# Kernel tuning notes

Measured on AMD Instinct MI355X. Metric: run time of the kernel, lower is better.

The kernel has to match this reference:

```python
import jax, jax.numpy as jnp
import numpy as np
from jax import lax

D_STATE = 16
D_CONV = 4
EXPAND = 2


def setup_inputs() -> dict:
    key = jax.random.key(0)
    ks = jax.random.split(key, 12)
    B, C, H, W = 8, 192, 32, 32
    d_inner = EXPAND * C            # 384
    dt_rank = (C + 15) // 16        # 12
    s = lambda k, shape, sc=0.02: jax.random.normal(k, shape, jnp.float32) * sc
    return {
        "x": jax.random.normal(ks[0], (B, C, H, W), jnp.float32),
        # proj_in: 1x1 Conv2d (in_ch -> out_ch)
        "proj_w": s(ks[1], (C, C)),
        "proj_b": s(ks[2], (C,)),
        # Mamba params (mamba_ssm defaults, biases per reference impl)
        "in_proj_w": s(ks[3], (2 * d_inner, C)),
        "conv_w": s(ks[4], (d_inner, D_CONV)),
        "conv_b": s(ks[5], (d_inner,)),
        "xproj_w": s(ks[6], (dt_rank + 2 * D_STATE, d_inner)),
        "dtproj_w": s(ks[7], (d_inner, dt_rank), 0.1),
        "dtproj_b": s(ks[8], (d_inner,), 0.5),
        "A_log": jnp.log(jnp.tile(jnp.arange(1, D_STATE + 1, dtype=jnp.float32), (d_inner, 1))),
        "Dp": jnp.ones((d_inner,), jnp.float32),
        "out_w": s(ks[9], (C, d_inner)),
    }


def _forward(x, proj_w, proj_b, in_proj_w, conv_w, conv_b, xproj_w,
             dtproj_w, dtproj_b, A_log, Dp, out_w):
    B, C, H, W = x.shape
    L = H * W
    # proj_in (1x1 conv) + flatten 'b c h w -> b (h w) c'
    u = jnp.einsum('bchw,oc->bhwo', x, proj_w).reshape(B, L, -1) + proj_b
    # Mamba layer
    xz = u @ in_proj_w.T                      # [B,L,2*d_inner]
    xin, z = jnp.split(xz, 2, axis=-1)
    # causal depthwise conv1d (kernel D_CONV), truncated to L
    xp = jnp.pad(xin, ((0, 0), (D_CONV - 1, 0), (0, 0)))
    xc = conv_b + sum(conv_w[:, k] * xp[:, k:k + L, :] for k in range(D_CONV))
    xc = jax.nn.silu(xc)
    # input-dependent dt, B, C
    dt_rank = dtproj_w.shape[1]
    x_dbl = xc @ xproj_w.T                    # [B,L,dt_rank+2*n]
    dtr, Bt, Ct = jnp.split(x_dbl, [dt_rank, dt_rank + D_STATE], axis=-1)
    dt = jax.nn.softplus(dtr @ dtproj_w.T + dtproj_b)   # [B,L,d_inner]
    A = -jnp.exp(A_log)                       # [d_inner, n]
    deltaA = jnp.exp(dt[..., None] * A)                          # [B,L,d,n]
    dBx = dt[..., None] * Bt[:, :, None, :] * xc[..., None]      # [B,L,d,n]

    def step(h, ins):
        dA, dbx, ct = ins                      # [B,d,n],[B,d,n],[B,n]
        h = dA * h + dbx
        return h, jnp.einsum('bdn,bn->bd', h, ct)

    h0 = jnp.zeros((B, A.shape[0], D_STATE), xc.dtype)
    _, ys = lax.scan(step, h0, (deltaA.transpose(1, 0, 2, 3),
                                dBx.transpose(1, 0, 2, 3),
                                Ct.transpose(1, 0, 2)))
    y = ys.transpose(1, 0, 2) + xc * Dp        # [B,L,d_inner]
    y = y * jax.nn.silu(z)
    out = y @ out_w.T                          # [B,L,C]
    # 'b (h w) c -> b c h w'
    return out.reshape(B, H, W, C).transpose(0, 3, 1, 2)


def reference(x, proj_w, proj_b, in_proj_w, conv_w, conv_b, xproj_w,
              dtproj_w, dtproj_b, A_log, Dp, out_w):
    return _forward(x, proj_w, proj_b, in_proj_w, conv_w, conv_b, xproj_w,
                    dtproj_w, dtproj_b, A_log, Dp, out_w)
```

## Files before the change

### kernel.cpp

```cpp
#include <hip/hip_runtime.h>
#include <math.h>

#define BB 8
#define CC 192
#define LL 1024
#define RT 8192
#define DI 384
#define DT_RANK 12
#define NS 16
#define NSEG 16
#define SEGL 64

typedef __attribute__((ext_vector_type(8))) short bf16x8;
typedef __attribute__((ext_vector_type(4))) float f32x4;

__device__ __forceinline__ unsigned short f2bf(float f) {
    unsigned u = __float_as_uint(f);
    unsigned r = (u + 0x7FFFu + ((u >> 16) & 1u)) >> 16;
    return (unsigned short)r;
}
__device__ __forceinline__ float bf2f(unsigned short h) {
    return __uint_as_float(((unsigned)h) << 16);
}

__device__ __forceinline__ float row_sum16(float v) {
    v += __int_as_float(__builtin_amdgcn_update_dpp(0, __float_as_int(v), 0x140, 0xF, 0xF, true));
    v += __int_as_float(__builtin_amdgcn_update_dpp(0, __float_as_int(v), 0x141, 0xF, 0xF, true));
    v += __int_as_float(__builtin_amdgcn_update_dpp(0, __float_as_int(v), 0x4E,  0xF, 0xF, true));
    v += __int_as_float(__builtin_amdgcn_update_dpp(0, __float_as_int(v), 0xB1,  0xF, 0xF, true));
    return v;
}

__global__ void fuse_w_kernel(const float* __restrict__ in_proj_w,
                              const float* __restrict__ proj_w,
                              const float* __restrict__ proj_b,
                              const float* __restrict__ out_w,
                              unsigned short* __restrict__ W2hi,
                              unsigned short* __restrict__ W2lo,
                              unsigned short* __restrict__ owhi,
                              unsigned short* __restrict__ owlo,
                              float* __restrict__ bias2,
                              float* __restrict__ xdT) {
    int j = blockIdx.x;
    int cp = threadIdx.x;
    int gtid = j * CC + cp;
    for (int i = gtid; i < 44 * RT; i += 768 * CC) xdT[i] = 0.f;
    if (j < DI) {
        float v = out_w[cp * DI + j];
        unsigned short h = f2bf(v);
        owhi[cp * DI + j] = h;
        owlo[cp * DI + j] = f2bf(v - bf2f(h));
    }
    __shared__ float wrow[CC];
    wrow[cp] = in_proj_w[j * CC + cp];
    __syncthreads();
    float acc = 0.f;
#pragma unroll 4
    for (int c = 0; c < CC; ++c) acc = fmaf(wrow[c], proj_w[c * CC + cp], acc);
    unsigned short h = f2bf(acc);
    W2hi[j * CC + cp] = h;
    W2lo[j * CC + cp] = f2bf(acc - bf2f(h));
    if (cp == 0) {
        float b = 0.f;
        for (int c = 0; c < CC; ++c) b = fmaf(wrow[c], proj_b[c], b);
        bias2[j] = b;
    }
}

__global__ __launch_bounds__(256) void gemm_xz(const float* __restrict__ x,
                                               const unsigned short* __restrict__ W2hi,
                                               const unsigned short* __restrict__ W2lo,
                                               const float* __restrict__ bias2,
                                               float* __restrict__ xzT) {
    __shared__ unsigned short xhi[2048];
    __shared__ unsigned short xlo[2048];
    int r0 = blockIdx.x * 64;
    int j0 = blockIdx.y * 64;
    int b  = r0 >> 10;
    int l0 = r0 & 1023;
    int tid = threadIdx.x;
    int lane = tid & 63;
    int wid = tid >> 6;
    int jw = j0 + wid * 16;
    const float* xb = x + b * CC * LL + l0 + lane;
    f32x4 z4 = {0.f, 0.f, 0.f, 0.f};
    f32x4 acc[4] = {z4, z4, z4, z4};
    int arow = jw + (lane & 15);
    int akb  = (lane >> 4) * 8;
    for (int ks = 0; ks < 6; ++ks) {
        int k0 = ks * 32;
        float v[8];
#pragma unroll
        for (int e = 0; e < 8; ++e) v[e] = xb[(k0 + wid * 8 + e) * LL];
        union U8 { unsigned short u[8]; bf16x8 v8; } hv, lv;
#pragma unroll
        for (int e = 0; e < 8; ++e) {
            unsigned short h = f2bf(v[e]);
            hv.u[e] = h;
            lv.u[e] = f2bf(v[e] - bf2f(h));
        }
        *(bf16x8*)&xhi[(wid * 64 + lane) * 8] = hv.v8;
        *(bf16x8*)&xlo[(wid * 64 + lane) * 8] = lv.v8;
        __syncthreads();
        int aoff = arow * CC + k0 + akb;
        bf16x8 ah = *(const bf16x8*)&W2hi[aoff];
        bf16x8 al = *(const bf16x8*)&W2lo[aoff];
#pragma unroll
        for (int rt = 0; rt < 4; ++rt) {
            int boff = ((lane >> 4) * 64 + rt * 16 + (lane & 15)) * 8;
            bf16x8 bh = *(const bf16x8*)&xhi[boff];
            bf16x8 bl = *(const bf16x8*)&xlo[boff];
            acc[rt] = __builtin_amdgcn_mfma_f32_16x16x32_bf16(ah, bh, acc[rt], 0, 0, 0);
            acc[rt] = __builtin_amdgcn_mfma_f32_16x16x32_bf16(ah, bl, acc[rt], 0, 0, 0);
            acc[rt] = __builtin_amdgcn_mfma_f32_16x16x32_bf16(al, bh, acc[rt], 0, 0, 0);
        }
        __syncthreads();
    }
    bool is_z = (j0 >= DI);
#pragma unroll
    for (int rt = 0; rt < 4; ++rt) {
        int rbase = r0 + rt * 16 + (lane & 15);
#pragma unroll
        for (int reg = 0; reg < 4; ++reg) {
            int j = jw + (lane >> 4) * 4 + reg;
            float o = acc[rt][reg] + bias2[j];
            if (is_z) o = __fdividef(o, 1.f + __expf(-o));
            xzT[j * RT + rbase] = o;
        }
    }
}

__global__ __launch_bounds__(512) void xproj_conv_gemm(const float* __restrict__ xzT,
                                                       const float* __restrict__ conv_w,
                                                       const float* __restrict__ conv_b,
                                                       const float* __restrict__ aw,
                                                       float* __restrict__ xcT,
                                                       float* __restrict__ xdT) {
    __shared__ float Bs[32][64];
    int col0 = blockIdx.x * 64;
    int kbase = blockIdx.y * 192;
    int tid = threadIdx.x;
    int col = tid & 63, mg = tid >> 6;
    int mb = mg * 6;
    const float* ar[6];
#pragma unroll
    for (int m = 0; m < 6; ++m) ar[m] = aw + min(mb + m, 43) * DI + kbase;
    float acc[6] = {};
    int ks = tid >> 4, c4 = (tid & 15) * 4;
    bool atL0 = ((col0 & 1023) == 0) && (c4 == 0);
    for (int k0 = 0; k0 < 192; k0 += 32) {
        int dch = kbase + k0 + ks;
        const float* src = xzT + (size_t)dch * RT + col0 + c4;
        float4 cur = *(const float4*)src;
        float4 prev = make_float4(0.f, 0.f, 0.f, 0.f);
        if (!atL0) prev = *(const float4*)(src - 4);
        float4 w4 = *(const float4*)&conv_w[dch * 4];
        float bb = conv_b[dch];
        float v0 = bb + w4.w * cur.x + w4.z * prev.w + w4.y * prev.z + w4.x * prev.y;
        float v1 = bb + w4.w * cur.y + w4.z * cur.x  + w4.y * prev.w + w4.x * prev.z;
        float v2 = bb + w4.w * cur.z + w4.z * cur.y  + w4.y * cur.x  + w4.x * prev.w;
        float v3 = bb + w4.w * cur.w + w4.z * cur.z  + w4.y * cur.y  + w4.x * cur.x;
        float4 o;
        o.x = __fdividef(v0, 1.f + __expf(-v0));
        o.y = __fdividef(v1, 1.f + __expf(-v1));
        o.z = __fdividef(v2, 1.f + __expf(-v2));
        o.w = __fdividef(v3, 1.f + __expf(-v3));
        *(float4*)&Bs[ks][c4] = o;
        *(float4*)&xcT[(size_t)dch * RT + col0 + c4] = o;
        __syncthreads();
#pragma unroll
        for (int k = 0; k < 32; ++k) {
            float bv = Bs[k][col];
#pragma unroll
            for (int m = 0; m < 6; ++m)
                acc[m] = fmaf(ar[m][k0 + k], bv, acc[m]);
        }
        __syncthreads();
    }
#pragma unroll
    for (int m = 0; m < 6; ++m)
        if (mb + m < 44)
            atomicAdd(&xdT[(mb + m) * RT + col0 + col], acc[m]);
}

__global__ __launch_bounds__(256) void scan_part1(const float* __restrict__ xdT,
                                                  const float* __restrict__ xcT,
                                                  const float* __restrict__ dtw,
                                                  const float* __restrict__ dtb,
                                                  const float* __restrict__ A_log,
                                                  float* __restrict__ P,
                                                  float* __restrict__ Hf) {
    __shared__ float dt_s[16][20], g_s[16][20], B_s[16][20];
    __shared__ float dtr_s[12][17];
    __shared__ float dtw_s[192];
    __shared__ float dtb_s[16];
    int seg = blockIdx.x, d0 = blockIdx.y * 16, b = blockIdx.z;
    int row0 = b * LL + seg * SEGL;
    int tid = threadIdx.x;
    int lane = tid & 63;
    int n = lane & 15;
    int dl = ((tid >> 6) << 2) | (lane >> 4);
    int tdd = tid >> 4, ti = tid & 15;
    if (tid < 192) dtw_s[tid] = dtw[d0 * DT_RANK + tid];
    if (tid < 16)  dtb_s[tid] = dtb[d0 + tid];
    float a = -__expf(A_log[(d0 + dl) * NS + n]);
    float h = 0.f, sdt = 0.f;
    for (int ch = 0; ch < 4; ++ch) {
        int r = row0 + ch * 16;
        float xv = xcT[(d0 + tdd) * RT + r + ti];
        B_s[tdd][ti] = xdT[(12 + tdd) * RT + r + ti];
        if (tid < 192) dtr_s[tid >> 4][ti] = xdT[(tid >> 4) * RT + r + ti];
        __syncthreads();
        float acc = dtb_s[tdd];
#pragma unroll
        for (int rr = 0; rr < DT_RANK; ++rr)
            acc = fmaf(dtr_s[rr][ti], dtw_s[tdd * DT_RANK + rr], acc);
        float dtv = fmaxf(acc, 0.f) + __logf(1.f + __expf(-fabsf(acc)));
        dt_s[tdd][ti] = dtv;
        g_s[tdd][ti]  = dtv * xv;
        __syncthreads();
        float dv[16], gb[16];
#pragma unroll
        for (int q = 0; q < 4; ++q) {
            float4 d4 = *(const float4*)&dt_s[dl][q * 4];
            float4 g4 = *(const float4*)&g_s[dl][q * 4];
            float4 b4 = *(const float4*)&B_s[n][q * 4];
            dv[q * 4 + 0] = d4.x; dv[q * 4 + 1] = d4.y;
            dv[q * 4 + 2] = d4.z; dv[q * 4 + 3] = d4.w;
            gb[q * 4 + 0] = g4.x * b4.x; gb[q * 4 + 1] = g4.y * b4.y;
            gb[q * 4 + 2] = g4.z * b4.z; gb[q * 4 + 3] = g4.w * b4.w;
        }
        __syncthreads();
        float eh[16];
#pragma unroll
        for (int i = 0; i < 16; ++i) eh[i] = __expf(dv[i] * a);
#pragma unroll
        for (int i = 0; i < 16; ++i) {
            sdt += dv[i];
            h = fmaf(eh[i], h, gb[i]);
        }
    }
    int idx = ((seg * BB + b) * DI + d0 + dl) * NS + n;
    P[idx] = __expf(a * sdt);
    Hf[idx] = h;
}

__global__ __launch_bounds__(256) void scan_part2(const float* __restrict__ xdT,
                                                  const float* __restrict__ xcT,
                                                  const float* __restrict__ zsT,
                                                  const float* __restrict__ dtw,
                                                  const float* __restrict__ dtb,
                                                  const float* __restrict__ P,
                                                  const float* __restrict__ Hf,
                                                  const float* __restrict__ A_log,
                                                  const float* __restrict__ Dp,
                                                  float* __restrict__ yT) {
    __shared__ float dt_s[16][20], g_s[16][20], B_s[16][20], C_s[16][20];
    __shared__ float dtr_s[12][17];
    __shared__ float dtw_s[192];
    __shared__ float dtb_s[16];
    int seg = blockIdx.x, d0 = blockIdx.y * 16, b = blockIdx.z;
    int row0 = b * LL + seg * SEGL;
    int tid = threadIdx.x;
    int lane = tid & 63;
    int n = lane & 15;
    int dl = ((tid >> 6) << 2) | (lane >> 4);
    int d = d0 + dl;
    int tdd = tid >> 4, ti = tid & 15;
    if (tid < 192) dtw_s[tid] = dtw[d0 * DT_RANK + tid];
    if (tid < 16)  dtb_s[tid] = dtb[d0 + tid];
    float a = -__expf(A_log[d * NS + n]);
    float Dpd = Dp[d];
    float h = 0.f;
    for (int s = 0; s < seg; ++s) {
        int off = ((s * BB + b) * DI + d) * NS + n;
        h = fmaf(P[off], h, Hf[off]);
    }
    for (int ch = 0; ch < 4; ++ch) {
        int r = row0 + ch * 16;
        float xr = xcT[(size_t)d * RT + r + n];
        float zr = zsT[(size_t)d * RT + r + n];
        float xv = xcT[(d0 + tdd) * RT + r + ti];
        B_s[tdd][ti] = xdT[(12 + tdd) * RT + r + ti];
        C_s[tdd][ti] = xdT[(28 + tdd) * RT + r + ti];
        if (tid < 192) dtr_s[tid >> 4][ti] = xdT[(tid >> 4) * RT + r + ti];
        __syncthreads();
        float acc = dtb_s[tdd];
#pragma unroll
        for (int rr = 0; rr < DT_RANK; ++rr)
            acc = fmaf(dtr_s[rr][ti], dtw_s[tdd * DT_RANK + rr], acc);
        float dtv = fmaxf(acc, 0.f) + __logf(1.f + __expf(-fabsf(acc)));
        dt_s[tdd][ti] = dtv;
        g_s[tdd][ti]  = dtv * xv;
        __syncthreads();
        float dv[16], gb[16], cv[16];
#pragma unroll
        for (int q = 0; q < 4; ++q) {
            float4 d4 = *(const float4*)&dt_s[dl][q * 4];
            float4 g4 = *(const float4*)&g_s[dl][q * 4];
            float4 b4 = *(const float4*)&B_s[n][q * 4];
            float4 c4 = *(const float4*)&C_s[n][q * 4];
            dv[q * 4 + 0] = d4.x; dv[q * 4 + 1] = d4.y;
            dv[q * 4 + 2] = d4.z; dv[q * 4 + 3] = d4.w;
            gb[q * 4 + 0] = g4.x * b4.x; gb[q * 4 + 1] = g4.y * b4.y;
            gb[q * 4 + 2] = g4.z * b4.z; gb[q * 4 + 3] = g4.w * b4.w;
            cv[q * 4 + 0] = c4.x; cv[q * 4 + 1] = c4.y;
            cv[q * 4 + 2] = c4.z; cv[q * 4 + 3] = c4.w;
        }
        __syncthreads();
        float eh[16];
#pragma unroll
        for (int i = 0; i < 16; ++i) eh[i] = __expf(dv[i] * a);
        float yacc = 0.f;
#pragma unroll
        for (int i = 0; i < 16; ++i) {
            h = fmaf(eh[i], h, gb[i]);
            float v = row_sum16(h * cv[i]);
            yacc = (n == i) ? v : yacc;
        }
        yT[(size_t)d * RT + r + n] = fmaf(xr, Dpd, yacc) * zr;
    }
}

__global__ __launch_bounds__(256) void gemm_out(const float* __restrict__ yT,
                                                const unsigned short* __restrict__ owhi,
                                                const unsigned short* __restrict__ owlo,
                                                float* __restrict__ out) {
    __shared__ unsigned short yhi[2048];
    __shared__ unsigned short ylo[2048];
    int r0 = blockIdx.x * 64;
    int c0 = blockIdx.y * 64;
    int b  = r0 >> 10;
    int l0 = r0 & 1023;
    int tid = threadIdx.x;
    int lane = tid & 63;
    int wid = tid >> 6;
    int cw = c0 + wid * 16;
    const float* yb = yT + r0 + lane;
    f32x4 z4 = {0.f, 0.f, 0.f, 0.f};
    f32x4 acc[4] = {z4, z4, z4, z4};
    int arow = cw + (lane & 15);
    int akb  = (lane >> 4) * 8;
    for (int ks = 0; ks < 12; ++ks) {
        int k0 = ks * 32;
        float v[8];
#pragma unroll
        for (int e = 0; e < 8; ++e) v[e] = yb[(size_t)(k0 + wid * 8 + e) * RT];
        union U8 { unsigned short u[8]; bf16x8 v8; } hv, lv;
#pragma unroll
        for (int e = 0; e < 8; ++e) {
            unsigned short h = f2bf(v[e]);
            hv.u[e] = h;
            lv.u[e] = f2bf(v[e] - bf2f(h));
        }
        *(bf16x8*)&yhi[(wid * 64 + lane) * 8] = hv.v8;
        *(bf16x8*)&ylo[(wid * 64 + lane) * 8] = lv.v8;
        __syncthreads();
        int aoff = arow * DI + k0 + akb;
        bf16x8 ah = *(const bf16x8*)&owhi[aoff];
        bf16x8 al = *(const bf16x8*)&owlo[aoff];
#pragma unroll
        for (int rt = 0; rt < 4; ++rt) {
            int boff = ((lane >> 4) * 64 + rt * 16 + (lane & 15)) * 8;
            bf16x8 bh = *(const bf16x8*)&yhi[boff];
            bf16x8 bl = *(const bf16x8*)&ylo[boff];
            acc[rt] = __builtin_amdgcn_mfma_f32_16x16x32_bf16(ah, bh, acc[rt], 0, 0, 0);
            acc[rt] = __builtin_amdgcn_mfma_f32_16x16x32_bf16(ah, bl, acc[rt], 0, 0, 0);
            acc[rt] = __builtin_amdgcn_mfma_f32_16x16x32_bf16(al, bh, acc[rt], 0, 0, 0);
        }
        __syncthreads();
    }
    float* ob = out + b * CC * LL;
#pragma unroll
    for (int rt = 0; rt < 4; ++rt) {
        int lbase = l0 + rt * 16 + (lane & 15);
#pragma unroll
        for (int reg = 0; reg < 4; ++reg) {
            int c = cw + (lane >> 4) * 4 + reg;
            ob[c * LL + lbase] = acc[rt][reg];
        }
    }
}

extern "C" void kernel_launch(void* const* d_in, const int* in_sizes, int n_in,
                              void* d_out, int out_size, void* d_ws, size_t ws_size,
                              hipStream_t stream) {
    const float* x         = (const float*)d_in[0];
    const float* proj_w    = (const float*)d_in[1];
    const float* proj_b    = (const float*)d_in[2];
    const float* in_proj_w = (const float*)d_in[3];
    const float* conv_w    = (const float*)d_in[4];
    const float* conv_b    = (const float*)d_in[5];
    const float* xproj_w   = (const float*)d_in[6];
    const float* dtproj_w  = (const float*)d_in[7];
    const float* dtproj_b  = (const float*)d_in[8];
    const float* A_log     = (const float*)d_in[9];
    const float* Dp        = (const float*)d_in[10];
    const float* out_w     = (const float*)d_in[11];
    float* out = (float*)d_out;

    float* ws    = (float*)d_ws;
    unsigned short* W2hi = (unsigned short*)ws;
    unsigned short* W2lo = (unsigned short*)(ws + 73728);
    float* bias2 = ws + 147456;
    float* xzT   = bias2 + 768;
    float* xcT   = xzT + 6291456;
    float* yT    = xcT + 3145728;
    float* xdT   = yT + 3145728;
    float* P     = xdT + 360448;
    float* Hf    = P + 786432;
    unsigned short* owhi = (unsigned short*)(Hf + 786432);
    unsigned short* owlo = (unsigned short*)(Hf + 786432 + 36864);
    float* zsT   = xzT + DI * RT;

    fuse_w_kernel<<<768, 192, 0, stream>>>(in_proj_w, proj_w, proj_b, out_w,
                                           W2hi, W2lo, owhi, owlo, bias2, xdT);
    gemm_xz<<<dim3(128, 12), 256, 0, stream>>>(x, W2hi, W2lo, bias2, xzT);
    xproj_conv_gemm<<<dim3(128, 2), 512, 0, stream>>>(xzT, conv_w, conv_b,
                                                      xproj_w, xcT, xdT);
    scan_part1<<<dim3(16, 24, 8), 256, 0, stream>>>(xdT, xcT, dtproj_w, dtproj_b,
                                                    A_log, P, Hf);
    scan_part2<<<dim3(16, 24, 8), 256, 0, stream>>>(xdT, xcT, zsT, dtproj_w, dtproj_b,
                                                    P, Hf, A_log, Dp, yT);
    gemm_out<<<dim3(128, 3), 256, 0, stream>>>(yT, owhi, owlo, out);
}
```

Measured before the change: 202.2 us.

## Replace two-pass segmented scan with single-pass sequential scan with register prefetch

Merges the segmented two-kernel selective scan into one kernel where each block scans the full sequence for 16 channels of one batch, dropping the per-segment state/decay intermediates and the recomputation in the first pass. Next-chunk inputs are prefetched into registers to hide global load latency, and one barrier per chunk is removed. This trades away segment-level parallelism, leaving only 192 blocks with a long serial dependency chain per block.

```diff
diff --git a/kernel.cpp b/kernel.cpp
--- a/kernel.cpp
+++ b/kernel.cpp
@@ -8,8 +8,6 @@
 #define DI 384
 #define DT_RANK 12
 #define NS 16
-#define NSEG 16
-#define SEGL 64
 
 typedef __attribute__((ext_vector_type(8))) short bf16x8;
 typedef __attribute__((ext_vector_type(4))) float f32x4;
@@ -183,84 +181,20 @@
             atomicAdd(&xdT[(mb + m) * RT + col0 + col], acc[m]);
 }
 
-__global__ __launch_bounds__(256) void scan_part1(const float* __restrict__ xdT,
-                                                  const float* __restrict__ xcT,
-                                                  const float* __restrict__ dtw,
-                                                  const float* __restrict__ dtb,
-                                                  const float* __restrict__ A_log,
-                                                  float* __restrict__ P,
-                                                  float* __restrict__ Hf) {
-    __shared__ float dt_s[16][20], g_s[16][20], B_s[16][20];
-    __shared__ float dtr_s[12][17];
-    __shared__ float dtw_s[192];
-    __shared__ float dtb_s[16];
-    int seg = blockIdx.x, d0 = blockIdx.y * 16, b = blockIdx.z;
-    int row0 = b * LL + seg * SEGL;
-    int tid = threadIdx.x;
-    int lane = tid & 63;
-    int n = lane & 15;
-    int dl = ((tid >> 6) << 2) | (lane >> 4);
-    int tdd = tid >> 4, ti = tid & 15;
-    if (tid < 192) dtw_s[tid] = dtw[d0 * DT_RANK + tid];
-    if (tid < 16)  dtb_s[tid] = dtb[d0 + tid];
-    float a = -__expf(A_log[(d0 + dl) * NS + n]);
-    float h = 0.f, sdt = 0.f;
-    for (int ch = 0; ch < 4; ++ch) {
-        int r = row0 + ch * 16;
-        float xv = xcT[(d0 + tdd) * RT + r + ti];
-        B_s[tdd][ti] = xdT[(12 + tdd) * RT + r + ti];
-        if (tid < 192) dtr_s[tid >> 4][ti] = xdT[(tid >> 4) * RT + r + ti];
-        __syncthreads();
-        float acc = dtb_s[tdd];
-#pragma unroll
-        for (int rr = 0; rr < DT_RANK; ++rr)
-            acc = fmaf(dtr_s[rr][ti], dtw_s[tdd * DT_RANK + rr], acc);
-        float dtv = fmaxf(acc, 0.f) + __logf(1.f + __expf(-fabsf(acc)));
-        dt_s[tdd][ti] = dtv;
-        g_s[tdd][ti]  = dtv * xv;
-        __syncthreads();
-        float dv[16], gb[16];
-#pragma unroll
-        for (int q = 0; q < 4; ++q) {
-            float4 d4 = *(const float4*)&dt_s[dl][q * 4];
-            float4 g4 = *(const float4*)&g_s[dl][q * 4];
-            float4 b4 = *(const float4*)&B_s[n][q * 4];
-            dv[q * 4 + 0] = d4.x; dv[q * 4 + 1] = d4.y;
-            dv[q * 4 + 2] = d4.z; dv[q * 4 + 3] = d4.w;
-            gb[q * 4 + 0] = g4.x * b4.x; gb[q * 4 + 1] = g4.y * b4.y;
-            gb[q * 4 + 2] = g4.z * b4.z; gb[q * 4 + 3] = g4.w * b4.w;
-        }
-        __syncthreads();
-        float eh[16];
-#pragma unroll
-        for (int i = 0; i < 16; ++i) eh[i] = __expf(dv[i] * a);
-#pragma unroll
-        for (int i = 0; i < 16; ++i) {
-            sdt += dv[i];
-            h = fmaf(eh[i], h, gb[i]);
-        }
-    }
-    int idx = ((seg * BB + b) * DI + d0 + dl) * NS + n;
-    P[idx] = __expf(a * sdt);
-    Hf[idx] = h;
-}
-
-__global__ __launch_bounds__(256) void scan_part2(const float* __restrict__ xdT,
-                                                  const float* __restrict__ xcT,
-                                                  const float* __restrict__ zsT,
-                                                  const float* __restrict__ dtw,
-                                                  const float* __restrict__ dtb,
-                                                  const float* __restrict__ P,
-                                                  const float* __restrict__ Hf,
-                                                  const float* __restrict__ A_log,
-                                                  const float* __restrict__ Dp,
-                                                  float* __restrict__ yT) {
+__global__ __launch_bounds__(256) void scan_full(const float* __restrict__ xdT,
+                                                 const float* __restrict__ xcT,
+                                                 const float* __restrict__ zsT,
+                                                 const float* __restrict__ dtw,
+                                                 const float* __restrict__ dtb,
+                                                 const float* __restrict__ A_log,
+                                                 const float* __restrict__ Dp,
+                                                 float* __restrict__ yT) {
     __shared__ float dt_s[16][20], g_s[16][20], B_s[16][20], C_s[16][20];
     __shared__ float dtr_s[12][17];
     __shared__ float dtw_s[192];
     __shared__ float dtb_s[16];
-    int seg = blockIdx.x, d0 = blockIdx.y * 16, b = blockIdx.z;
-    int row0 = b * LL + seg * SEGL;
+    int d0 = blockIdx.x * 16, b = blockIdx.y;
+    int row0 = b * LL;
     int tid = threadIdx.x;
     int lane = tid & 63;
     int n = lane & 15;
@@ -272,26 +206,34 @@
     float a = -__expf(A_log[d * NS + n]);
     float Dpd = Dp[d];
     float h = 0.f;
-    for (int s = 0; s < seg; ++s) {
-        int off = ((s * BB + b) * DI + d) * NS + n;
-        h = fmaf(P[off], h, Hf[off]);
-    }
-    for (int ch = 0; ch < 4; ++ch) {
+    float xv  = xcT[(d0 + tdd) * RT + row0 + ti];
+    float bvp = xdT[(12 + tdd) * RT + row0 + ti];
+    float cvp = xdT[(28 + tdd) * RT + row0 + ti];
+    float dtrv = (tid < 192) ? xdT[(tid >> 4) * RT + row0 + ti] : 0.f;
+    float xr = xcT[(size_t)d * RT + row0 + n];
+    float zr = zsT[(size_t)d * RT + row0 + n];
+    for (int ch = 0; ch < 64; ++ch) {
         int r = row0 + ch * 16;
-        float xr = xcT[(size_t)d * RT + r + n];
-        float zr = zsT[(size_t)d * RT + r + n];
-        float xv = xcT[(d0 + tdd) * RT + r + ti];
-        B_s[tdd][ti] = xdT[(12 + tdd) * RT + r + ti];
-        C_s[tdd][ti] = xdT[(28 + tdd) * RT + r + ti];
-        if (tid < 192) dtr_s[tid >> 4][ti] = xdT[(tid >> 4) * RT + r + ti];
-        __syncthreads();
+        __syncthreads();
+        B_s[tdd][ti] = bvp;
+        C_s[tdd][ti] = cvp;
+        if (tid < 192) dtr_s[tid >> 4][ti] = dtrv;
+        float xv_c = xv, xr_c = xr, zr_c = zr;
+        __syncthreads();
+        int rn = row0 + min(ch + 1, 63) * 16;
+        xv  = xcT[(d0 + tdd) * RT + rn + ti];
+        bvp = xdT[(12 + tdd) * RT + rn + ti];
+        cvp = xdT[(28 + tdd) * RT + rn + ti];
+        if (tid < 192) dtrv = xdT[(tid >> 4) * RT + rn + ti];
+        xr = xcT[(size_t)d * RT + rn + n];
+        zr = zsT[(size_t)d * RT + rn + n];
         float acc = dtb_s[tdd];
 #pragma unroll
         for (int rr = 0; rr < DT_RANK; ++rr)
             acc = fmaf(dtr_s[rr][ti], dtw_s[tdd * DT_RANK + rr], acc);
         float dtv = fmaxf(acc, 0.f) + __logf(1.f + __expf(-fabsf(acc)));
         dt_s[tdd][ti] = dtv;
-        g_s[tdd][ti]  = dtv * xv;
+        g_s[tdd][ti]  = dtv * xv_c;
         __syncthreads();
         float dv[16], gb[16], cv[16];
 #pragma unroll
@@ -307,7 +249,6 @@
             cv[q * 4 + 0] = c4.x; cv[q * 4 + 1] = c4.y;
             cv[q * 4 + 2] = c4.z; cv[q * 4 + 3] = c4.w;
         }
-        __syncthreads();
         float eh[16];
 #pragma unroll
         for (int i = 0; i < 16; ++i) eh[i] = __expf(dv[i] * a);
@@ -318,7 +259,7 @@
             float v = row_sum16(h * cv[i]);
             yacc = (n == i) ? v : yacc;
         }
-        yT[(size_t)d * RT + r + n] = fmaf(xr, Dpd, yacc) * zr;
+        yT[(size_t)d * RT + r + n] = fmaf(xr_c, Dpd, yacc) * zr_c;
     }
 }
 
@@ -407,10 +348,8 @@
     float* xcT   = xzT + 6291456;
     float* yT    = xcT + 3145728;
     float* xdT   = yT + 3145728;
-    float* P     = xdT + 360448;
-    float* Hf    = P + 786432;
-    unsigned short* owhi = (unsigned short*)(Hf + 786432);
-    unsigned short* owlo = (unsigned short*)(Hf + 786432 + 36864);
+    unsigned short* owhi = (unsigned short*)(xdT + 360448);
+    unsigned short* owlo = (unsigned short*)(xdT + 360448 + 36864);
     float* zsT   = xzT + DI * RT;
 
     fuse_w_kernel<<<768, 192, 0, stream>>>(in_proj_w, proj_w, proj_b, out_w,
@@ -418,9 +357,7 @@
     gemm_xz<<<dim3(128, 12), 256, 0, stream>>>(x, W2hi, W2lo, bias2, xzT);
     xproj_conv_gemm<<<dim3(128, 2), 512, 0, stream>>>(xzT, conv_w, conv_b,
                                                       xproj_w, xcT, xdT);
-    scan_part1<<<dim3(16, 24, 8), 256, 0, stream>>>(xdT, xcT, dtproj_w, dtproj_b,
-                                                    A_log, P, Hf);
-    scan_part2<<<dim3(16, 24, 8), 256, 0, stream>>>(xdT, xcT, zsT, dtproj_w, dtproj_b,
-                                                    P, Hf, A_log, Dp, yT);
+    scan_full<<<dim3(24, 8), 256, 0, stream>>>(xdT, xcT, zsT, dtproj_w, dtproj_b,
+                                               A_log, Dp, yT);
     gemm_out<<<dim3(128, 3), 256, 0, stream>>>(yT, owhi, owlo, out);
 }
```

New measurement: 218.9 us. 8.3% more time.

## Precompute dt and dt*x in separate kernel, drop shared-memory staging in scans

Applied to the files above, without the earlier changes.

Adds a dt_g_kernel that computes softplus(dt projection) and dt*xc once per element and writes them to global buffers dtT and gT. Both scan kernels then read dt, g, B and C directly from global memory with float4 loads instead of recomputing dt through shared memory, which removes their block-wide barriers. This avoids computing dt twice and the sync overhead in the scans, at the cost of an extra launch and about 25 MB of additional global writes and reads. The workspace layout is rearranged to hold the new buffers.

```diff
diff --git a/kernel.cpp b/kernel.cpp
--- a/kernel.cpp
+++ b/kernel.cpp
@@ -183,54 +183,67 @@
             atomicAdd(&xdT[(mb + m) * RT + col0 + col], acc[m]);
 }
 
-__global__ __launch_bounds__(256) void scan_part1(const float* __restrict__ xdT,
-                                                  const float* __restrict__ xcT,
-                                                  const float* __restrict__ dtw,
-                                                  const float* __restrict__ dtb,
+__global__ __launch_bounds__(256) void dt_g_kernel(const float* __restrict__ xdT,
+                                                   const float* __restrict__ xcT,
+                                                   const float* __restrict__ dtw,
+                                                   const float* __restrict__ dtb,
+                                                   float* __restrict__ dtT,
+                                                   float* __restrict__ gT) {
+    __shared__ float dtw_s[192];
+    __shared__ float dtb_s[16];
+    int tid = threadIdx.x;
+    int row = blockIdx.x * 256 + tid;
+    int d0 = blockIdx.y * 16;
+    if (tid < 192) dtw_s[tid] = dtw[d0 * DT_RANK + tid];
+    if (tid < 16)  dtb_s[tid] = dtb[d0 + tid];
+    __syncthreads();
+    float dtr[DT_RANK];
+#pragma unroll
+    for (int rr = 0; rr < DT_RANK; ++rr) dtr[rr] = xdT[rr * RT + row];
+#pragma unroll
+    for (int dd = 0; dd < 16; ++dd) {
+        int d = d0 + dd;
+        float acc = dtb_s[dd];
+#pragma unroll
+        for (int rr = 0; rr < DT_RANK; ++rr)
+            acc = fmaf(dtr[rr], dtw_s[dd * DT_RANK + rr], acc);
+        float dtv = fmaxf(acc, 0.f) + __logf(1.f + __expf(-fabsf(acc)));
+        dtT[(size_t)d * RT + row] = dtv;
+        gT[(size_t)d * RT + row]  = dtv * xcT[(size_t)d * RT + row];
+    }
+}
+
+__global__ __launch_bounds__(256) void scan_part1(const float* __restrict__ dtT,
+                                                  const float* __restrict__ gT,
+                                                  const float* __restrict__ xdT,
                                                   const float* __restrict__ A_log,
                                                   float* __restrict__ P,
                                                   float* __restrict__ Hf) {
-    __shared__ float dt_s[16][20], g_s[16][20], B_s[16][20];
-    __shared__ float dtr_s[12][17];
-    __shared__ float dtw_s[192];
-    __shared__ float dtb_s[16];
     int seg = blockIdx.x, d0 = blockIdx.y * 16, b = blockIdx.z;
     int row0 = b * LL + seg * SEGL;
     int tid = threadIdx.x;
     int lane = tid & 63;
     int n = lane & 15;
     int dl = ((tid >> 6) << 2) | (lane >> 4);
-    int tdd = tid >> 4, ti = tid & 15;
-    if (tid < 192) dtw_s[tid] = dtw[d0 * DT_RANK + tid];
-    if (tid < 16)  dtb_s[tid] = dtb[d0 + tid];
-    float a = -__expf(A_log[(d0 + dl) * NS + n]);
+    int d = d0 + dl;
+    float a = -__expf(A_log[d * NS + n]);
     float h = 0.f, sdt = 0.f;
     for (int ch = 0; ch < 4; ++ch) {
         int r = row0 + ch * 16;
-        float xv = xcT[(d0 + tdd) * RT + r + ti];
-        B_s[tdd][ti] = xdT[(12 + tdd) * RT + r + ti];
-        if (tid < 192) dtr_s[tid >> 4][ti] = xdT[(tid >> 4) * RT + r + ti];
-        __syncthreads();
-        float acc = dtb_s[tdd];
-#pragma unroll
-        for (int rr = 0; rr < DT_RANK; ++rr)
-            acc = fmaf(dtr_s[rr][ti], dtw_s[tdd * DT_RANK + rr], acc);
-        float dtv = fmaxf(acc, 0.f) + __logf(1.f + __expf(-fabsf(acc)));
-        dt_s[tdd][ti] = dtv;
-        g_s[tdd][ti]  = dtv * xv;
-        __syncthreads();
+        const float4* dt4 = (const float4*)&dtT[(size_t)d * RT + r];
+        const float4* g4p = (const float4*)&gT[(size_t)d * RT + r];
+        const float4* b4p = (const float4*)&xdT[(size_t)(12 + n) * RT + r];
         float dv[16], gb[16];
 #pragma unroll
         for (int q = 0; q < 4; ++q) {
-            float4 d4 = *(const float4*)&dt_s[dl][q * 4];
-            float4 g4 = *(const float4*)&g_s[dl][q * 4];
-            float4 b4 = *(const float4*)&B_s[n][q * 4];
+            float4 d4 = dt4[q];
+            float4 g4 = g4p[q];
+            float4 b4 = b4p[q];
             dv[q * 4 + 0] = d4.x; dv[q * 4 + 1] = d4.y;
             dv[q * 4 + 2] = d4.z; dv[q * 4 + 3] = d4.w;
             gb[q * 4 + 0] = g4.x * b4.x; gb[q * 4 + 1] = g4.y * b4.y;
             gb[q * 4 + 2] = g4.z * b4.z; gb[q * 4 + 3] = g4.w * b4.w;
         }
-        __syncthreads();
         float eh[16];
 #pragma unroll
         for (int i = 0; i < 16; ++i) eh[i] = __expf(dv[i] * a);
@@ -240,25 +253,21 @@
             h = fmaf(eh[i], h, gb[i]);
         }
     }
-    int idx = ((seg * BB + b) * DI + d0 + dl) * NS + n;
+    int idx = ((seg * BB + b) * DI + d) * NS + n;
     P[idx] = __expf(a * sdt);
     Hf[idx] = h;
 }
 
-__global__ __launch_bounds__(256) void scan_part2(const float* __restrict__ xdT,
+__global__ __launch_bounds__(256) void scan_part2(const float* __restrict__ dtT,
+                                                  const float* __restrict__ gT,
+                                                  const float* __restrict__ xdT,
                                                   const float* __restrict__ xcT,
                                                   const float* __restrict__ zsT,
-                                                  const float* __restrict__ dtw,
-                                                  const float* __restrict__ dtb,
                                                   const float* __restrict__ P,
                                                   const float* __restrict__ Hf,
                                                   const float* __restrict__ A_log,
                                                   const float* __restrict__ Dp,
                                                   float* __restrict__ yT) {
-    __shared__ float dt_s[16][20], g_s[16][20], B_s[16][20], C_s[16][20];
-    __shared__ float dtr_s[12][17];
-    __shared__ float dtw_s[192];
-    __shared__ float dtb_s[16];
     int seg = blockIdx.x, d0 = blockIdx.y * 16, b = blockIdx.z;
     int row0 = b * LL + seg * SEGL;
     int tid = threadIdx.x;
@@ -266,9 +275,6 @@
     int n = lane & 15;
     int dl = ((tid >> 6) << 2) | (lane >> 4);
     int d = d0 + dl;
-    int tdd = tid >> 4, ti = tid & 15;
-    if (tid < 192) dtw_s[tid] = dtw[d0 * DT_RANK + tid];
-    if (tid < 16)  dtb_s[tid] = dtb[d0 + tid];
     float a = -__expf(A_log[d * NS + n]);
     float Dpd = Dp[d];
     float h = 0.f;
@@ -278,28 +284,19 @@
     }
     for (int ch = 0; ch < 4; ++ch) {
         int r = row0 + ch * 16;
+        const float4* dt4 = (const float4*)&dtT[(size_t)d * RT + r];
+        const float4* g4p = (const float4*)&gT[(size_t)d * RT + r];
+        const float4* b4p = (const float4*)&xdT[(size_t)(12 + n) * RT + r];
+        const float4* c4p = (const float4*)&xdT[(size_t)(28 + n) * RT + r];
         float xr = xcT[(size_t)d * RT + r + n];
         float zr = zsT[(size_t)d * RT + r + n];
-        float xv = xcT[(d0 + tdd) * RT + r + ti];
-        B_s[tdd][ti] = xdT[(12 + tdd) * RT + r + ti];
-        C_s[tdd][ti] = xdT[(28 + tdd) * RT + r + ti];
-        if (tid < 192) dtr_s[tid >> 4][ti] = xdT[(tid >> 4) * RT + r + ti];
-        __syncthreads();
-        float acc = dtb_s[tdd];
-#pragma unroll
-        for (int rr = 0; rr < DT_RANK; ++rr)
-            acc = fmaf(dtr_s[rr][ti], dtw_s[tdd * DT_RANK + rr], acc);
-        float dtv = fmaxf(acc, 0.f) + __logf(1.f + __expf(-fabsf(acc)));
-        dt_s[tdd][ti] = dtv;
-        g_s[tdd][ti]  = dtv * xv;
-        __syncthreads();
         float dv[16], gb[16], cv[16];
 #pragma unroll
         for (int q = 0; q < 4; ++q) {
-            float4 d4 = *(const float4*)&dt_s[dl][q * 4];
-            float4 g4 = *(const float4*)&g_s[dl][q * 4];
-            float4 b4 = *(const float4*)&B_s[n][q * 4];
-            float4 c4 = *(const float4*)&C_s[n][q * 4];
+            float4 d4 = dt4[q];
+            float4 g4 = g4p[q];
+            float4 b4 = b4p[q];
+            float4 c4 = c4p[q];
             dv[q * 4 + 0] = d4.x; dv[q * 4 + 1] = d4.y;
             dv[q * 4 + 2] = d4.z; dv[q * 4 + 3] = d4.w;
             gb[q * 4 + 0] = g4.x * b4.x; gb[q * 4 + 1] = g4.y * b4.y;
@@ -307,7 +304,6 @@
             cv[q * 4 + 0] = c4.x; cv[q * 4 + 1] = c4.y;
             cv[q * 4 + 2] = c4.z; cv[q * 4 + 3] = c4.w;
         }
-        __syncthreads();
         float eh[16];
 #pragma unroll
         for (int i = 0; i < 16; ++i) eh[i] = __expf(dv[i] * a);
@@ -407,10 +403,12 @@
     float* xcT   = xzT + 6291456;
     float* yT    = xcT + 3145728;
     float* xdT   = yT + 3145728;
-    float* P     = xdT + 360448;
+    unsigned short* owhi = (unsigned short*)(xdT + 360448);
+    unsigned short* owlo = (unsigned short*)(xdT + 360448 + 36864);
+    float* dtT   = xdT + 360448 + 73728;
+    float* gT    = dtT + 3145728;
+    float* P     = gT + 3145728;
     float* Hf    = P + 786432;
-    unsigned short* owhi = (unsigned short*)(Hf + 786432);
-    unsigned short* owlo = (unsigned short*)(Hf + 786432 + 36864);
     float* zsT   = xzT + DI * RT;
 
     fuse_w_kernel<<<768, 192, 0, stream>>>(in_proj_w, proj_w, proj_b, out_w,
@@ -418,9 +416,10 @@
     gemm_xz<<<dim3(128, 12), 256, 0, stream>>>(x, W2hi, W2lo, bias2, xzT);
     xproj_conv_gemm<<<dim3(128, 2), 512, 0, stream>>>(xzT, conv_w, conv_b,
                                                       xproj_w, xcT, xdT);
-    scan_part1<<<dim3(16, 24, 8), 256, 0, stream>>>(xdT, xcT, dtproj_w, dtproj_b,
-                                                    A_log, P, Hf);
-    scan_part2<<<dim3(16, 24, 8), 256, 0, stream>>>(xdT, xcT, zsT, dtproj_w, dtproj_b,
+    dt_g_kernel<<<dim3(32, 24), 256, 0, stream>>>(xdT, xcT, dtproj_w, dtproj_b,
+                                                  dtT, gT);
+    scan_part1<<<dim3(16, 24, 8), 256, 0, stream>>>(dtT, gT, xdT, A_log, P, Hf);
+    scan_part2<<<dim3(16, 24, 8), 256, 0, stream>>>(dtT, gT, xdT, xcT, zsT,
                                                     P, Hf, A_log, Dp, yT);
     gemm_out<<<dim3(128, 3), 256, 0, stream>>>(yT, owhi, owlo, out);
 }
```

Measured after the change: 258.0 us. 1.28x slower.
